# Kernel optimization log

Measured on AMD Instinct MI355X. Metric: run time of the kernel, lower is better.

## Reference

```python
import jax, jax.numpy as jnp
import numpy as np

NUM_USERS = 100000
NUM_ITEMS = 50000
N_NODES = NUM_USERS + NUM_ITEMS
LATENT_DIM = 64
XIJ_DIM = 16
N_LAYERS = 3
NNZ = 6400000
BATCH = 8192


def setup_inputs() -> dict:
    key = jax.random.key(0)
    ks = jax.random.split(key, 12)
    return {
        "emb_user": jax.random.normal(ks[0], (NUM_USERS, LATENT_DIM), jnp.float32),
        "emb_item": jax.random.normal(ks[1], (NUM_ITEMS, LATENT_DIM), jnp.float32),
        "emb_user_xij": jax.random.normal(ks[2], (NUM_USERS, XIJ_DIM), jnp.float32),
        "emb_item_xij1": jax.random.normal(ks[3], (NUM_ITEMS, XIJ_DIM), jnp.float32),
        "emb_item_xij0": jax.random.normal(ks[4], (NUM_ITEMS, XIJ_DIM), jnp.float32),
        "w_user": jax.random.normal(ks[5], (1,), jnp.float32),
        "w_item": jax.random.normal(ks[6], (1,), jnp.float32),
        "graph_vals": jax.random.uniform(ks[7], (NNZ,), jnp.float32),
        "graph_rows": jax.random.randint(ks[8], (NNZ,), 0, N_NODES, jnp.int64).astype(jnp.int32),
        "graph_cols": jax.random.randint(ks[9], (NNZ,), 0, N_NODES, jnp.int64).astype(jnp.int32),
        "users": jax.random.randint(ks[10], (BATCH,), 0, NUM_USERS, jnp.int64).astype(jnp.int32),
        "items": jax.random.randint(ks[11], (BATCH,), 0, NUM_ITEMS, jnp.int64).astype(jnp.int32),
        "xij": jax.random.randint(jax.random.fold_in(key, 99), (BATCH,), 0, 2, jnp.int32),
    }


def _spmm(rows, cols, vals, x):
    # y[r] = sum_{e: rows[e]==r} vals[e] * x[cols[e]]
    return jax.ops.segment_sum(vals[:, None] * x[cols], rows, num_segments=N_NODES)


def reference(emb_user, emb_item, emb_user_xij, emb_item_xij1, emb_item_xij0,
              w_user, w_item, graph_vals, graph_rows, graph_cols,
              users, items, xij):
    # LightGCN propagation with running-mean accumulator (fuses the stack+mean)
    all_emb = jnp.concatenate([emb_user, emb_item], axis=0)  # [N, D]
    acc = all_emb
    for _ in range(N_LAYERS):
        all_emb = _spmm(graph_rows, graph_cols, graph_vals, all_emb)
        acc = acc + all_emb
    light_out = acc / (N_LAYERS + 1)
    all_users = light_out[:NUM_USERS]
    all_items = light_out[NUM_USERS:]

    users_emb = w_user * all_users[users]          # [B, D]
    items_emb = w_item * all_items[items]          # [B, D]
    xij_user_emb = emb_user_xij[users]             # [B, Dx]
    xij_item_emb = jnp.where(xij[:, None].astype(bool),
                             emb_item_xij1[items], emb_item_xij0[items])

    users_mix = jax.nn.softmax(jnp.concatenate([users_emb, xij_user_emb], axis=1), axis=1)
    items_mix = jax.nn.sigmoid(jnp.concatenate([items_emb, xij_item_emb], axis=1))
    gamma = jnp.sum(users_mix * items_mix, axis=1)  # [B]
    return gamma
```

## Files before the change

### kernel.cpp

```cpp
#include <hip/hip_runtime.h>
#include <hip/hip_bf16.h>
#include <hip/hip_fp16.h>
#include <math.h>

#define NUM_USERS 100000
#define NUM_ITEMS 50000
#define N_NODES   150000
#define DIM       64
#define VAL_SCALE 16383.0f
#define VAL_INV   (1.0f / 16383.0f)

#define SSHIFT 9
#define SROWS  512
#define NBS    ((N_NODES + SROWS - 1) / SROWS)
#define CAP    16
#define FLUSH  8
#define SCAT_WGS 1280
#define GPAD   16
#define SLOTS  32768
#define PKSLOTS 22744
#define SENTINEL 0xFFFFFFFFu
#define BBT 512

__global__ void copy_init_kernel(const float4* __restrict__ eu, const float4* __restrict__ ei,
                                 ushort4* __restrict__ cur, int total4) {
    int i = blockIdx.x * blockDim.x + threadIdx.x;
    if (i >= total4) return;
    const int user_lim = NUM_USERS * (DIM / 4);
    float4 v = (i < user_lim) ? eu[i] : ei[i - user_lim];
    ushort4 h;
    h.x = __half_as_ushort(__float2half_rn(v.x));
    h.y = __half_as_ushort(__float2half_rn(v.y));
    h.z = __half_as_ushort(__float2half_rn(v.z));
    h.w = __half_as_ushort(__float2half_rn(v.w));
    cur[i] = h;
}

__global__ void gcur_init_kernel(int* __restrict__ gcur) {
    int b = blockIdx.x * blockDim.x + threadIdx.x;
    if (b < NBS) gcur[b * GPAD] = b * SLOTS;
}

__global__ __launch_bounds__(256) void binned_scatter_kernel(
        const int* __restrict__ rows, const int* __restrict__ cols,
        const float* __restrict__ vals, int* __restrict__ gcur,
        uint2* __restrict__ pk8, int nnz) {
    __shared__ unsigned       lbufA[NBS * CAP];
    __shared__ unsigned short lbufB[NBS * CAP];
    __shared__ int            lcur[NBS];
    int t = threadIdx.x;
    for (int i = t; i < NBS; i += 256) lcur[i] = 0;
    __syncthreads();

    int per_wg = (((nnz + (int)gridDim.x - 1) / (int)gridDim.x) + 1) & ~1;
    int e0 = blockIdx.x * per_wg;
    int e1 = min(e0 + per_wg, nnz);

    for (int base = e0; base < e1; base += 512) {
        int e = base + t * 2;
        if (e + 1 < e1) {
            int2   r2 = *(const int2*)(rows + e);
            int2   c2 = *(const int2*)(cols + e);
            float2 v2 = *(const float2*)(vals + e);
            #pragma unroll
            for (int k = 0; k < 2; ++k) {
                int r = k ? r2.y : r2.x;
                unsigned q = __float2uint_rn((k ? v2.y : v2.x) * VAL_SCALE);
                unsigned ax = (unsigned)(k ? c2.y : c2.x) | (q << 18);
                int b = r >> SSHIFT;
                int pos = atomicAdd(&lcur[b], 1);
                if (pos < CAP) {
                    lbufA[b * CAP + pos] = ax;
                    lbufB[b * CAP + pos] = (unsigned short)(r - (b << SSHIFT));
                } else {
                    atomicSub(&lcur[b], 1);
                    int p = atomicAdd(&gcur[b * GPAD], 8);
                    *(uint4*)(&pk8[p])     = make_uint4(ax, (unsigned)r, 0u, SENTINEL);
                    *(uint4*)(&pk8[p + 2]) = make_uint4(0u, SENTINEL, 0u, SENTINEL);
                    *(uint4*)(&pk8[p + 4]) = make_uint4(0u, SENTINEL, 0u, SENTINEL);
                    *(uint4*)(&pk8[p + 6]) = make_uint4(0u, SENTINEL, 0u, SENTINEL);
                }
            }
        } else if (e < e1) {
            int r = rows[e];
            unsigned q = __float2uint_rn(vals[e] * VAL_SCALE);
            unsigned ax = (unsigned)cols[e] | (q << 18);
            int b = r >> SSHIFT;
            int pos = atomicAdd(&lcur[b], 1);
            if (pos < CAP) {
                lbufA[b * CAP + pos] = ax;
                lbufB[b * CAP + pos] = (unsigned short)(r - (b << SSHIFT));
            } else {
                atomicSub(&lcur[b], 1);
                int p = atomicAdd(&gcur[b * GPAD], 8);
                *(uint4*)(&pk8[p])     = make_uint4(ax, (unsigned)r, 0u, SENTINEL);
                *(uint4*)(&pk8[p + 2]) = make_uint4(0u, SENTINEL, 0u, SENTINEL);
                *(uint4*)(&pk8[p + 4]) = make_uint4(0u, SENTINEL, 0u, SENTINEL);
                *(uint4*)(&pk8[p + 6]) = make_uint4(0u, SENTINEL, 0u, SENTINEL);
            }
        }
        __syncthreads();
        for (int b2 = t; b2 < NBS; b2 += 256) {
            int c = lcur[b2];
            if (c >= FLUSH) {
                int ng = c >> 3;
                int p = atomicAdd(&gcur[b2 * GPAD], ng * 8);
                unsigned rbase = (unsigned)(b2 << SSHIFT);
                for (int j = 0; j < ng * 8; j += 2) {
                    uint4 q = make_uint4(lbufA[b2 * CAP + j],     rbase + lbufB[b2 * CAP + j],
                                         lbufA[b2 * CAP + j + 1], rbase + lbufB[b2 * CAP + j + 1]);
                    *(uint4*)(&pk8[p + j]) = q;
                }
                int rem = c - ng * 8;
                for (int j = 0; j < rem; ++j) {
                    lbufA[b2 * CAP + j] = lbufA[b2 * CAP + ng * 8 + j];
                    lbufB[b2 * CAP + j] = lbufB[b2 * CAP + ng * 8 + j];
                }
                lcur[b2] = rem;
            }
        }
        __syncthreads();
    }
    for (int b2 = t; b2 < NBS; b2 += 256) {
        int c = lcur[b2];
        if (c > 0) {
            int p = atomicAdd(&gcur[b2 * GPAD], 8);
            unsigned rbase = (unsigned)(b2 << SSHIFT);
            for (int j = 0; j < 8; j += 2) {
                unsigned a0 = (j     < c) ? lbufA[b2 * CAP + j]     : 0u;
                unsigned b0 = (j     < c) ? rbase + lbufB[b2 * CAP + j]     : SENTINEL;
                unsigned a1 = (j + 1 < c) ? lbufA[b2 * CAP + j + 1] : 0u;
                unsigned b1 = (j + 1 < c) ? rbase + lbufB[b2 * CAP + j + 1] : SENTINEL;
                *(uint4*)(&pk8[p + j]) = make_uint4(a0, b0, a1, b1);
            }
        }
    }
}

__global__ __launch_bounds__(BBT) void bucket_build_kernel(const int* __restrict__ gcur,
                                                           const uint2* __restrict__ pk8,
                                                           unsigned* __restrict__ pk,
                                                           int* __restrict__ rowbeg,
                                                           int* __restrict__ rowend) {
    __shared__ int lc[SROWS];
    __shared__ int ps[SROWS];
    int b  = blockIdx.x;
    int r0 = b * SROWS;
    int nr = min(r0 + SROWS, N_NODES) - r0;
    int t  = threadIdx.x;
    lc[t] = 0;
    __syncthreads();

    const uint4* p4 = (const uint4*)pk8;
    int i0   = (b * SLOTS) >> 1;
    int iend = gcur[b * GPAD] >> 1;

    #define CNT(q) { \
        if ((q).y != SENTINEL) atomicAdd(&lc[(int)(q).y - r0], 1); \
        if ((q).w != SENTINEL) atomicAdd(&lc[(int)(q).w - r0], 1); }

    int i = i0 + t;
    for (; i + 3 * BBT < iend; i += 4 * BBT) {
        uint4 qa = p4[i], qb = p4[i + BBT], qc = p4[i + 2 * BBT], qd = p4[i + 3 * BBT];
        CNT(qa) CNT(qb) CNT(qc) CNT(qd)
    }
    for (; i < iend; i += BBT) { uint4 qa = p4[i]; CNT(qa) }
    __syncthreads();

    int c = lc[t];
    ps[t] = c;
    __syncthreads();
    #pragma unroll
    for (int off = 1; off < SROWS; off <<= 1) {
        int u = (t >= off) ? ps[t - off] : 0;
        __syncthreads();
        ps[t] += u;
        __syncthreads();
    }
    int base = b * PKSLOTS + ps[t] - c;
    if (t < nr) { rowbeg[r0 + t] = base; rowend[r0 + t] = base + c; }
    lc[t] = base;
    __syncthreads();

    #define PLC(q) { \
        if ((q).y != SENTINEL) { int p_ = atomicAdd(&lc[(int)(q).y - r0], 1); pk[p_] = (q).x; } \
        if ((q).w != SENTINEL) { int p_ = atomicAdd(&lc[(int)(q).w - r0], 1); pk[p_] = (q).z; } }

    i = i0 + t;
    for (; i + 3 * BBT < iend; i += 4 * BBT) {
        uint4 qa = p4[i], qb = p4[i + BBT], qc = p4[i + 2 * BBT], qd = p4[i + 3 * BBT];
        PLC(qa) PLC(qb) PLC(qc) PLC(qd)
    }
    for (; i < iend; i += BBT) { uint4 qa = p4[i]; PLC(qa) }
}

__device__ __forceinline__ float row_pull(const int* __restrict__ rowbeg,
                                          const int* __restrict__ rowend,
                                          const unsigned* __restrict__ pk,
                                          const __half* __restrict__ x,
                                          int row, int lane) {
    int s0 = rowbeg[row];
    int s1 = rowend[row];
    float acc = 0.f;
    int e = s0;
    for (; e + 16 <= s1; e += 16) {
        unsigned p0 = pk[e + 0],  p1 = pk[e + 1],  p2 = pk[e + 2],  p3 = pk[e + 3];
        unsigned p4 = pk[e + 4],  p5 = pk[e + 5],  p6 = pk[e + 6],  p7 = pk[e + 7];
        unsigned p8 = pk[e + 8],  p9 = pk[e + 9],  pA = pk[e + 10], pB = pk[e + 11];
        unsigned pC = pk[e + 12], pD = pk[e + 13], pE = pk[e + 14], pF = pk[e + 15];
        float x0 = __half2float(x[((p0 & 0x3FFFFu) << 6) + lane]);
        float x1 = __half2float(x[((p1 & 0x3FFFFu) << 6) + lane]);
        float x2 = __half2float(x[((p2 & 0x3FFFFu) << 6) + lane]);
        float x3 = __half2float(x[((p3 & 0x3FFFFu) << 6) + lane]);
        float x4 = __half2float(x[((p4 & 0x3FFFFu) << 6) + lane]);
        float x5 = __half2float(x[((p5 & 0x3FFFFu) << 6) + lane]);
        float x6 = __half2float(x[((p6 & 0x3FFFFu) << 6) + lane]);
        float x7 = __half2float(x[((p7 & 0x3FFFFu) << 6) + lane]);
        float x8 = __half2float(x[((p8 & 0x3FFFFu) << 6) + lane]);
        float x9 = __half2float(x[((p9 & 0x3FFFFu) << 6) + lane]);
        float xA = __half2float(x[((pA & 0x3FFFFu) << 6) + lane]);
        float xB = __half2float(x[((pB & 0x3FFFFu) << 6) + lane]);
        float xC = __half2float(x[((pC & 0x3FFFFu) << 6) + lane]);
        float xD = __half2float(x[((pD & 0x3FFFFu) << 6) + lane]);
        float xE = __half2float(x[((pE & 0x3FFFFu) << 6) + lane]);
        float xF = __half2float(x[((pF & 0x3FFFFu) << 6) + lane]);
        acc = fmaf((float)(p0 >> 18), x0, acc);
        acc = fmaf((float)(p1 >> 18), x1, acc);
        acc = fmaf((float)(p2 >> 18), x2, acc);
        acc = fmaf((float)(p3 >> 18), x3, acc);
        acc = fmaf((float)(p4 >> 18), x4, acc);
        acc = fmaf((float)(p5 >> 18), x5, acc);
        acc = fmaf((float)(p6 >> 18), x6, acc);
        acc = fmaf((float)(p7 >> 18), x7, acc);
        acc = fmaf((float)(p8 >> 18), x8, acc);
        acc = fmaf((float)(p9 >> 18), x9, acc);
        acc = fmaf((float)(pA >> 18), xA, acc);
        acc = fmaf((float)(pB >> 18), xB, acc);
        acc = fmaf((float)(pC >> 18), xC, acc);
        acc = fmaf((float)(pD >> 18), xD, acc);
        acc = fmaf((float)(pE >> 18), xE, acc);
        acc = fmaf((float)(pF >> 18), xF, acc);
    }
    for (; e + 8 <= s1; e += 8) {
        unsigned p0 = pk[e + 0], p1 = pk[e + 1], p2 = pk[e + 2], p3 = pk[e + 3];
        unsigned p4 = pk[e + 4], p5 = pk[e + 5], p6 = pk[e + 6], p7 = pk[e + 7];
        float x0 = __half2float(x[((p0 & 0x3FFFFu) << 6) + lane]);
        float x1 = __half2float(x[((p1 & 0x3FFFFu) << 6) + lane]);
        float x2 = __half2float(x[((p2 & 0x3FFFFu) << 6) + lane]);
        float x3 = __half2float(x[((p3 & 0x3FFFFu) << 6) + lane]);
        float x4 = __half2float(x[((p4 & 0x3FFFFu) << 6) + lane]);
        float x5 = __half2float(x[((p5 & 0x3FFFFu) << 6) + lane]);
        float x6 = __half2float(x[((p6 & 0x3FFFFu) << 6) + lane]);
        float x7 = __half2float(x[((p7 & 0x3FFFFu) << 6) + lane]);
        acc = fmaf((float)(p0 >> 18), x0, acc);
        acc = fmaf((float)(p1 >> 18), x1, acc);
        acc = fmaf((float)(p2 >> 18), x2, acc);
        acc = fmaf((float)(p3 >> 18), x3, acc);
        acc = fmaf((float)(p4 >> 18), x4, acc);
        acc = fmaf((float)(p5 >> 18), x5, acc);
        acc = fmaf((float)(p6 >> 18), x6, acc);
        acc = fmaf((float)(p7 >> 18), x7, acc);
    }
    for (; e < s1; ++e) {
        unsigned p = pk[e];
        acc = fmaf((float)(p >> 18), __half2float(x[((p & 0x3FFFFu) << 6) + lane]), acc);
    }
    return acc * VAL_INV;
}

__global__ __launch_bounds__(256) void pull_kernel(const int* __restrict__ rowbeg,
                                                   const int* __restrict__ rowend,
                                                   const unsigned* __restrict__ pk,
                                                   const __half* __restrict__ x,
                                                   __half* __restrict__ y) {
    int lane = threadIdx.x & 63;
    int wv   = __builtin_amdgcn_readfirstlane(threadIdx.x >> 6);
    int row  = blockIdx.x * 4 + wv;
    if (row >= N_NODES) return;
    float acc = row_pull(rowbeg, rowend, pk, x, row, lane);
    y[((size_t)row << 6) + lane] = __float2half_rn(acc);
}

__global__ __launch_bounds__(256) void tail_kernel(const int* __restrict__ rowbeg,
                                                   const int* __restrict__ rowend,
                                                   const unsigned* __restrict__ pk,
                                                   const __half* __restrict__ cur,
                                                   const __half* __restrict__ nxt,
                                                   const float* __restrict__ eu,
                                                   const float* __restrict__ ei,
                                                   const float* __restrict__ exu,
                                                   const float* __restrict__ exi1,
                                                   const float* __restrict__ exi0,
                                                   const float* __restrict__ w_user,
                                                   const float* __restrict__ w_item,
                                                   const int* __restrict__ users,
                                                   const int* __restrict__ items,
                                                   const int* __restrict__ xijf,
                                                   float* __restrict__ out, int batch) {
    int lane = threadIdx.x & 63;
    int wv   = blockIdx.x * 4 + __builtin_amdgcn_readfirstlane(threadIdx.x >> 6);
    if (wv >= batch) return;
    int u    = users[wv];
    int it   = items[wv];
    int xf   = xijf[wv];
    int rowU = u;
    int rowI = NUM_USERS + it;

    float l3u = row_pull(rowbeg, rowend, pk, cur, rowU, lane);
    float l3i = row_pull(rowbeg, rowend, pk, cur, rowI, lane);

    float wu = w_user[0] * 0.25f;
    float wi = w_item[0] * 0.25f;

    float su = eu[((size_t)u  << 6) + lane]
             + __half2float(nxt[((size_t)rowU << 6) + lane])
             + __half2float(cur[((size_t)rowU << 6) + lane])
             + l3u;
    float si = ei[((size_t)it << 6) + lane]
             + __half2float(nxt[((size_t)rowI << 6) + lane])
             + __half2float(cur[((size_t)rowI << 6) + lane])
             + l3i;
    float ua = wu * su;
    float ia = wi * si;

    float ub = -INFINITY, ib = 0.f;
    if (lane < 16) {
        ub = exu[(size_t)u * 16 + lane];
        ib = xf ? exi1[(size_t)it * 16 + lane] : exi0[(size_t)it * 16 + lane];
    }

    float m = fmaxf(ua, ub);
    #pragma unroll
    for (int off = 32; off; off >>= 1) m = fmaxf(m, __shfl_xor(m, off));
    float ea = expf(ua - m);
    float eb = (lane < 16) ? expf(ub - m) : 0.f;
    float s = ea + eb;
    #pragma unroll
    for (int off = 32; off; off >>= 1) s += __shfl_xor(s, off);
    float inv = 1.f / s;

    float sa = 1.f / (1.f + expf(-ia));
    float sb = (lane < 16) ? 1.f / (1.f + expf(-ib)) : 0.f;

    float g = ea * inv * sa + eb * inv * sb;
    #pragma unroll
    for (int off = 32; off; off >>= 1) g += __shfl_xor(g, off);
    if (lane == 0) out[wv] = g;
}

extern "C" void kernel_launch(void* const* d_in, const int* in_sizes, int n_in,
                              void* d_out, int out_size, void* d_ws, size_t ws_size,
                              hipStream_t stream) {
    const float* emb_user = (const float*)d_in[0];
    const float* emb_item = (const float*)d_in[1];
    const float* exu      = (const float*)d_in[2];
    const float* exi1     = (const float*)d_in[3];
    const float* exi0     = (const float*)d_in[4];
    const float* w_user   = (const float*)d_in[5];
    const float* w_item   = (const float*)d_in[6];
    const float* gvals    = (const float*)d_in[7];
    const int*   grows    = (const int*)d_in[8];
    const int*   gcols    = (const int*)d_in[9];
    const int*   users    = (const int*)d_in[10];
    const int*   items    = (const int*)d_in[11];
    const int*   xijf     = (const int*)d_in[12];
    float*       out      = (float*)d_out;

    const int nnz   = in_sizes[7];
    const int batch = in_sizes[10];

    const size_t node_elems = (size_t)N_NODES * DIM;
    const size_t PK8_BYTES  = (size_t)NBS * SLOTS * 8;
    char* w = (char*)d_ws;
    uint2*    pk8   = (uint2*)w;
    __half*   cur   = (__half*)w;
    __half*   nxt   = cur + node_elems;
    w += PK8_BYTES;
    unsigned* pk     = (unsigned*)w;              w += (size_t)NBS * PKSLOTS * 4;
    int*      rowbeg = (int*)w;                   w += (size_t)N_NODES * 4;
    int*      rowend = (int*)w;                   w += (size_t)N_NODES * 4;
    int*      gcur   = (int*)w;                   w += (size_t)NBS * GPAD * 4;

    const int tb = 256;
    const int total4 = N_NODES * (DIM / 4);

    gcur_init_kernel<<<(NBS + tb - 1) / tb, tb, 0, stream>>>(gcur);
    binned_scatter_kernel<<<SCAT_WGS, 256, 0, stream>>>(grows, gcols, gvals, gcur, pk8, nnz);
    bucket_build_kernel<<<NBS, BBT, 0, stream>>>(gcur, pk8, pk, rowbeg, rowend);

    copy_init_kernel<<<(total4 + tb - 1) / tb, tb, 0, stream>>>(
        (const float4*)emb_user, (const float4*)emb_item, (ushort4*)cur, total4);

    const int pull_blocks = (N_NODES + 3) / 4;
    const int tail_blocks = (batch + 3) / 4;

    pull_kernel<<<pull_blocks, tb, 0, stream>>>(rowbeg, rowend, pk, cur, nxt);
    pull_kernel<<<pull_blocks, tb, 0, stream>>>(rowbeg, rowend, pk, nxt, cur);
    tail_kernel<<<tail_blocks, tb, 0, stream>>>(
        rowbeg, rowend, pk, cur, nxt, emb_user, emb_item,
        exu, exi1, exi0, w_user, w_item, users, items, xijf, out, batch);
}
```

Before: 519.3 us.

## Build per-row histogram with global atomics during scatter, drop counting pass

The scatter kernel now increments a global per-row histogram with an atomic for every edge. The bucket build reads row counts from that histogram instead of making a separate counting pass over the binned records, which removes one full read of the pk8 buffer. The scatter loop also reads four edges per thread with vector loads instead of two. The cost is 6.4M scattered global atomics spread over 150K addresses, plus a histogram buffer and zeroing it in the init kernel.

```diff
diff --git a/kernel.cpp b/kernel.cpp
--- a/kernel.cpp
+++ b/kernel.cpp
@@ -36,15 +36,16 @@
     cur[i] = h;
 }
 
-__global__ void gcur_init_kernel(int* __restrict__ gcur) {
-    int b = blockIdx.x * blockDim.x + threadIdx.x;
-    if (b < NBS) gcur[b * GPAD] = b * SLOTS;
+__global__ void init_kernel(int* __restrict__ gcur, int* __restrict__ hist) {
+    int i = blockIdx.x * blockDim.x + threadIdx.x;
+    if (i < NBS) gcur[i * GPAD] = i * SLOTS;
+    if (i < N_NODES) hist[i] = 0;
 }
 
 __global__ __launch_bounds__(256) void binned_scatter_kernel(
         const int* __restrict__ rows, const int* __restrict__ cols,
         const float* __restrict__ vals, int* __restrict__ gcur,
-        uint2* __restrict__ pk8, int nnz) {
+        int* __restrict__ hist, uint2* __restrict__ pk8, int nnz) {
     __shared__ unsigned       lbufA[NBS * CAP];
     __shared__ unsigned short lbufB[NBS * CAP];
     __shared__ int            lcur[NBS];
@@ -52,51 +53,42 @@
     for (int i = t; i < NBS; i += 256) lcur[i] = 0;
     __syncthreads();
 
-    int per_wg = (((nnz + (int)gridDim.x - 1) / (int)gridDim.x) + 1) & ~1;
+    int per_wg = (((nnz + (int)gridDim.x - 1) / (int)gridDim.x) + 3) & ~3;
     int e0 = blockIdx.x * per_wg;
     int e1 = min(e0 + per_wg, nnz);
 
-    for (int base = e0; base < e1; base += 512) {
-        int e = base + t * 2;
-        if (e + 1 < e1) {
-            int2   r2 = *(const int2*)(rows + e);
-            int2   c2 = *(const int2*)(cols + e);
-            float2 v2 = *(const float2*)(vals + e);
-            #pragma unroll
-            for (int k = 0; k < 2; ++k) {
-                int r = k ? r2.y : r2.x;
-                unsigned q = __float2uint_rn((k ? v2.y : v2.x) * VAL_SCALE);
-                unsigned ax = (unsigned)(k ? c2.y : c2.x) | (q << 18);
-                int b = r >> SSHIFT;
-                int pos = atomicAdd(&lcur[b], 1);
-                if (pos < CAP) {
-                    lbufA[b * CAP + pos] = ax;
-                    lbufB[b * CAP + pos] = (unsigned short)(r - (b << SSHIFT));
-                } else {
-                    atomicSub(&lcur[b], 1);
-                    int p = atomicAdd(&gcur[b * GPAD], 8);
-                    *(uint4*)(&pk8[p])     = make_uint4(ax, (unsigned)r, 0u, SENTINEL);
-                    *(uint4*)(&pk8[p + 2]) = make_uint4(0u, SENTINEL, 0u, SENTINEL);
-                    *(uint4*)(&pk8[p + 4]) = make_uint4(0u, SENTINEL, 0u, SENTINEL);
-                    *(uint4*)(&pk8[p + 6]) = make_uint4(0u, SENTINEL, 0u, SENTINEL);
-                }
-            }
-        } else if (e < e1) {
-            int r = rows[e];
-            unsigned q = __float2uint_rn(vals[e] * VAL_SCALE);
-            unsigned ax = (unsigned)cols[e] | (q << 18);
-            int b = r >> SSHIFT;
-            int pos = atomicAdd(&lcur[b], 1);
-            if (pos < CAP) {
-                lbufA[b * CAP + pos] = ax;
-                lbufB[b * CAP + pos] = (unsigned short)(r - (b << SSHIFT));
-            } else {
-                atomicSub(&lcur[b], 1);
-                int p = atomicAdd(&gcur[b * GPAD], 8);
-                *(uint4*)(&pk8[p])     = make_uint4(ax, (unsigned)r, 0u, SENTINEL);
-                *(uint4*)(&pk8[p + 2]) = make_uint4(0u, SENTINEL, 0u, SENTINEL);
-                *(uint4*)(&pk8[p + 4]) = make_uint4(0u, SENTINEL, 0u, SENTINEL);
-                *(uint4*)(&pk8[p + 6]) = make_uint4(0u, SENTINEL, 0u, SENTINEL);
+    #define PROC(rr, cc, vv) { \
+        int r = (rr); \
+        unsigned q = __float2uint_rn((vv) * VAL_SCALE); \
+        unsigned ax = (unsigned)(cc) | (q << 18); \
+        atomicAdd(&hist[r], 1); \
+        int b = r >> SSHIFT; \
+        int pos = atomicAdd(&lcur[b], 1); \
+        if (pos < CAP) { \
+            lbufA[b * CAP + pos] = ax; \
+            lbufB[b * CAP + pos] = (unsigned short)(r - (b << SSHIFT)); \
+        } else { \
+            atomicSub(&lcur[b], 1); \
+            int p = atomicAdd(&gcur[b * GPAD], 8); \
+            *(uint4*)(&pk8[p])     = make_uint4(ax, (unsigned)r, 0u, SENTINEL); \
+            *(uint4*)(&pk8[p + 2]) = make_uint4(0u, SENTINEL, 0u, SENTINEL); \
+            *(uint4*)(&pk8[p + 4]) = make_uint4(0u, SENTINEL, 0u, SENTINEL); \
+            *(uint4*)(&pk8[p + 6]) = make_uint4(0u, SENTINEL, 0u, SENTINEL); \
+        } }
+
+    for (int base = e0; base < e1; base += 1024) {
+        int e = base + t * 4;
+        if (e + 3 < e1) {
+            int4   r4 = *(const int4*)(rows + e);
+            int4   c4 = *(const int4*)(cols + e);
+            float4 v4 = *(const float4*)(vals + e);
+            PROC(r4.x, c4.x, v4.x)
+            PROC(r4.y, c4.y, v4.y)
+            PROC(r4.z, c4.z, v4.z)
+            PROC(r4.w, c4.w, v4.w)
+        } else {
+            for (int ee = e; ee < e1 && ee < e + 4; ++ee) {
+                PROC(rows[ee], cols[ee], vals[ee])
             }
         }
         __syncthreads();
@@ -127,9 +119,9 @@
             int p = atomicAdd(&gcur[b2 * GPAD], 8);
             unsigned rbase = (unsigned)(b2 << SSHIFT);
             for (int j = 0; j < 8; j += 2) {
-                unsigned a0 = (j     < c) ? lbufA[b2 * CAP + j]     : 0u;
+                unsigned a0 = (j     < c) ? lbufA[b2 * CAP + j]             : 0u;
                 unsigned b0 = (j     < c) ? rbase + lbufB[b2 * CAP + j]     : SENTINEL;
-                unsigned a1 = (j + 1 < c) ? lbufA[b2 * CAP + j + 1] : 0u;
+                unsigned a1 = (j + 1 < c) ? lbufA[b2 * CAP + j + 1]         : 0u;
                 unsigned b1 = (j + 1 < c) ? rbase + lbufB[b2 * CAP + j + 1] : SENTINEL;
                 *(uint4*)(&pk8[p + j]) = make_uint4(a0, b0, a1, b1);
             }
@@ -138,6 +130,7 @@
 }
 
 __global__ __launch_bounds__(BBT) void bucket_build_kernel(const int* __restrict__ gcur,
+                                                           const int* __restrict__ hist,
                                                            const uint2* __restrict__ pk8,
                                                            unsigned* __restrict__ pk,
                                                            int* __restrict__ rowbeg,
@@ -148,26 +141,8 @@
     int r0 = b * SROWS;
     int nr = min(r0 + SROWS, N_NODES) - r0;
     int t  = threadIdx.x;
-    lc[t] = 0;
-    __syncthreads();
-
-    const uint4* p4 = (const uint4*)pk8;
-    int i0   = (b * SLOTS) >> 1;
-    int iend = gcur[b * GPAD] >> 1;
-
-    #define CNT(q) { \
-        if ((q).y != SENTINEL) atomicAdd(&lc[(int)(q).y - r0], 1); \
-        if ((q).w != SENTINEL) atomicAdd(&lc[(int)(q).w - r0], 1); }
-
-    int i = i0 + t;
-    for (; i + 3 * BBT < iend; i += 4 * BBT) {
-        uint4 qa = p4[i], qb = p4[i + BBT], qc = p4[i + 2 * BBT], qd = p4[i + 3 * BBT];
-        CNT(qa) CNT(qb) CNT(qc) CNT(qd)
-    }
-    for (; i < iend; i += BBT) { uint4 qa = p4[i]; CNT(qa) }
-    __syncthreads();
-
-    int c = lc[t];
+
+    int c = (t < nr) ? hist[r0 + t] : 0;
     ps[t] = c;
     __syncthreads();
     #pragma unroll
@@ -182,11 +157,15 @@
     lc[t] = base;
     __syncthreads();
 
+    const uint4* p4 = (const uint4*)pk8;
+    int i0   = (b * SLOTS) >> 1;
+    int iend = gcur[b * GPAD] >> 1;
+
     #define PLC(q) { \
         if ((q).y != SENTINEL) { int p_ = atomicAdd(&lc[(int)(q).y - r0], 1); pk[p_] = (q).x; } \
         if ((q).w != SENTINEL) { int p_ = atomicAdd(&lc[(int)(q).w - r0], 1); pk[p_] = (q).z; } }
 
-    i = i0 + t;
+    int i = i0 + t;
     for (; i + 3 * BBT < iend; i += 4 * BBT) {
         uint4 qa = p4[i], qb = p4[i + BBT], qc = p4[i + 2 * BBT], qd = p4[i + 3 * BBT];
         PLC(qa) PLC(qb) PLC(qc) PLC(qd)
@@ -380,13 +359,14 @@
     int*      rowbeg = (int*)w;                   w += (size_t)N_NODES * 4;
     int*      rowend = (int*)w;                   w += (size_t)N_NODES * 4;
     int*      gcur   = (int*)w;                   w += (size_t)NBS * GPAD * 4;
+    int*      hist   = (int*)w;                   w += (size_t)N_NODES * 4;
 
     const int tb = 256;
     const int total4 = N_NODES * (DIM / 4);
 
-    gcur_init_kernel<<<(NBS + tb - 1) / tb, tb, 0, stream>>>(gcur);
-    binned_scatter_kernel<<<SCAT_WGS, 256, 0, stream>>>(grows, gcols, gvals, gcur, pk8, nnz);
-    bucket_build_kernel<<<NBS, BBT, 0, stream>>>(gcur, pk8, pk, rowbeg, rowend);
+    init_kernel<<<(N_NODES + tb - 1) / tb, tb, 0, stream>>>(gcur, hist);
+    binned_scatter_kernel<<<SCAT_WGS, 256, 0, stream>>>(grows, gcols, gvals, gcur, hist, pk8, nnz);
+    bucket_build_kernel<<<NBS, BBT, 0, stream>>>(gcur, hist, pk8, pk, rowbeg, rowend);
 
     copy_init_kernel<<<(total4 + tb - 1) / tb, tb, 0, stream>>>(
         (const float4*)emb_user, (const float4*)emb_item, (ushort4*)cur, total4);
```

Result: slower. 731.3 us (+40.8%).
